# Performance work log

Hardware: AMD Instinct MI355X
Metric: run time of the kernel (lower is better)

## Reference

```python
import jax, jax.numpy as jnp
import numpy as np

NIN = 4096
NOUT = 4096
LN_EPS = 1e-5  # torch.nn.LayerNorm default


def setup_inputs() -> dict:
    key = jax.random.key(0)
    ks = jax.random.split(key, 8)
    x = jax.random.normal(ks[0], (1, NIN), dtype=jnp.float32)
    hid = jax.random.normal(ks[1], (1, NOUT), dtype=jnp.float32)
    hebb = jnp.zeros((NOUT, NOUT), dtype=jnp.float32) + 1e-6  # initialZeroHebb
    # parameters
    w_in = 0.01 * jax.random.normal(ks[2], (NOUT, NIN), dtype=jnp.float32)  # inp_lin weight (no bias)
    w = 0.01 * jnp.eye(NOUT, NOUT, dtype=jnp.float32)                        # Plastic.w
    alpha = 0.01 * jax.random.normal(ks[3], (NOUT, NOUT), dtype=jnp.float32)
    b = 0.01 * jax.random.normal(ks[4], (NOUT,), dtype=jnp.float32)
    lamda = 0.01 * jnp.ones((1,), dtype=jnp.float32)
    pred_eta = 0.01 * jax.random.normal(ks[5], (NOUT, NOUT), dtype=jnp.float32)
    pred_eta_b = 0.01 * jax.random.normal(ks[6], (NOUT,), dtype=jnp.float32)
    ln_gamma = jnp.ones((NOUT,), dtype=jnp.float32)
    ln_beta = jnp.zeros((NOUT,), dtype=jnp.float32)
    return {"x": x, "hid": hid, "hebb": hebb, "w_in": w_in, "w": w,
            "alpha": alpha, "b": b, "lamda": lamda, "pred_eta": pred_eta,
            "pred_eta_b": pred_eta_b, "ln_gamma": ln_gamma, "ln_beta": ln_beta}


def reference(x, hid, hebb, w_in, w, alpha, b, lamda, pred_eta, pred_eta_b, ln_gamma, ln_beta):
    # Cell.forward (nonlin = ReLU for both wx and the post-LN output)
    wx = jax.nn.relu(x @ w_in.T)                       # [1, nout]
    wh = hid @ (w + alpha * hebb) + b                  # Plastic.forward, [1, nout]
    s = wx + wh
    mu = jnp.mean(s, axis=-1, keepdims=True)
    var = jnp.mean((s - mu) ** 2, axis=-1, keepdims=True)
    ln = ln_gamma * (s - mu) * jax.lax.rsqrt(var + LN_EPS) + ln_beta
    wy = jax.nn.relu(ln)                               # new hidden state, [1, nout]
    # Plastic.update_hebb(x=hid, y=wh, hebb)
    eta_hat = jax.nn.sigmoid(wh @ pred_eta + pred_eta_b)           # [1, nout]
    outer = hid[0, :, None] * wh[0, None, :]                        # [nout, nout]
    hebb_new = (1.0 - lamda) * hebb + eta_hat.T * outer             # row i scaled by eta_hat[0, i]
    return wy, hebb_new
```

## Files before the change

kernel.cpp:

```cpp
#include <hip/hip_runtime.h>
#include <hip/hip_bf16.h>
#include <math.h>

#define N 4096
#define NGRP 16

typedef float f32x4 __attribute__((ext_vector_type(4)));

__inline__ __device__ float waveReduceSum(float v) {
    #pragma unroll
    for (int o = 32; o > 0; o >>= 1) v += __shfl_down(v, o);
    return v;
}

#define LD4(p, o) (*reinterpret_cast<const float4*>((p) + (o)))

__inline__ __device__ f32x4 ntld4(const float* p) {
    return __builtin_nontemporal_load(reinterpret_cast<const f32x4*>(p));
}

template<int ITERS>
__global__ __launch_bounds__(256) void k_sweep_wh_t(const float* __restrict__ hid,
                                                    const float* __restrict__ w,
                                                    const float* __restrict__ alpha,
                                                    const float* __restrict__ hebb,
                                                    float* __restrict__ part,
                                                    int G) {
    int b = blockIdx.x, t = threadIdx.x;
    int p = b >> 2;
    int j0 = (((b & 3) << 8) | t) * 4;
    int P = G >> 2;
    size_t step = (size_t)G * 1024;
    size_t off = (size_t)(((b << 8) | t)) * 4;

    f32x4 wv[ITERS], av[ITERS], bv[ITERS];
    float hv[ITERS];
    #pragma unroll
    for (int k = 0; k < ITERS; ++k) {
        size_t o = off + (size_t)k * step;
        wv[k] = ntld4(w + o);
        av[k] = ntld4(alpha + o);
        bv[k] = *reinterpret_cast<const f32x4*>(hebb + o);
    }
    #pragma unroll
    for (int k = 0; k < ITERS; ++k) hv[k] = hid[k * P + p];

    f32x4 acc = {0.f, 0.f, 0.f, 0.f};
    #pragma unroll
    for (int k = 0; k < ITERS; ++k) {
        float h = hv[k];
        acc.x = fmaf(h, fmaf(av[k].x, bv[k].x, wv[k].x), acc.x);
        acc.y = fmaf(h, fmaf(av[k].y, bv[k].y, wv[k].y), acc.y);
        acc.z = fmaf(h, fmaf(av[k].z, bv[k].z, wv[k].z), acc.z);
        acc.w = fmaf(h, fmaf(av[k].w, bv[k].w, wv[k].w), acc.w);
    }
    *reinterpret_cast<f32x4*>(part + (size_t)p * N + j0) = acc;
}

__global__ __launch_bounds__(256) void k_sweep_wh(const float* __restrict__ hid,
                                                  const float* __restrict__ w,
                                                  const float* __restrict__ alpha,
                                                  const float* __restrict__ hebb,
                                                  float* __restrict__ part,
                                                  int G, int iters) {
    int b = blockIdx.x, t = threadIdx.x;
    int p = b >> 2;
    int j0 = (((b & 3) << 8) | t) * 4;
    int P = G >> 2;
    float4 acc = make_float4(0.f, 0.f, 0.f, 0.f);
    size_t step = (size_t)G * 1024;
    size_t off = (size_t)(((b << 8) | t)) * 4;
    #pragma unroll 8
    for (int k = 0; k < iters; ++k, off += step) {
        float h = hid[k * P + p];
        float4 wv = LD4(w, off);
        float4 av = LD4(alpha, off);
        float4 hv = LD4(hebb, off);
        acc.x = fmaf(h, fmaf(av.x, hv.x, wv.x), acc.x);
        acc.y = fmaf(h, fmaf(av.y, hv.y, wv.y), acc.y);
        acc.z = fmaf(h, fmaf(av.z, hv.z, wv.z), acc.z);
        acc.w = fmaf(h, fmaf(av.w, hv.w, wv.w), acc.w);
    }
    *reinterpret_cast<float4*>(part + (size_t)p * N + j0) = acc;
}

__global__ __launch_bounds__(256) void k_red_wx(const float* __restrict__ part,
                                                float* __restrict__ part2,
                                                int cpg,
                                                const float* __restrict__ x,
                                                const float* __restrict__ w_in,
                                                float* __restrict__ wx_out,
                                                int nred) {
    int t = threadIdx.x;
    if ((int)blockIdx.x < nred) {
        int g  = blockIdx.x >> 2;
        int xt = blockIdx.x & 3;
        int j0 = (xt * 256 + t) * 4;
        const float4* p4 = reinterpret_cast<const float4*>(part);
        float4 s = make_float4(0.f, 0.f, 0.f, 0.f);
        #pragma unroll 8
        for (int c = 0; c < cpg; ++c) {
            float4 v = p4[((size_t)(g * cpg + c) * N + j0) >> 2];
            s.x += v.x; s.y += v.y; s.z += v.z; s.w += v.w;
        }
        *reinterpret_cast<float4*>(part2 + (size_t)g * N + j0) = s;
    } else {
        int j = blockIdx.x - nred;
        const float4* row = reinterpret_cast<const float4*>(w_in + (size_t)j * N);
        const float4* xv  = reinterpret_cast<const float4*>(x);
        float sum = 0.f;
        #pragma unroll
        for (int k = t; k < N / 4; k += 256) {
            float4 a = row[k], c = xv[k];
            sum += a.x * c.x + a.y * c.y + a.z * c.z + a.w * c.w;
        }
        sum = waveReduceSum(sum);
        __shared__ float wsum[4];
        int wid = t >> 6, lane = t & 63;
        if (lane == 0) wsum[wid] = sum;
        __syncthreads();
        if (t == 0)
            wx_out[j] = fmaxf(wsum[0] + wsum[1] + wsum[2] + wsum[3], 0.f);
    }
}

__global__ __launch_bounds__(1024) void k_ln(const float* __restrict__ part2,
                                             const float* __restrict__ wx,
                                             const float* __restrict__ b,
                                             const float* __restrict__ gamma,
                                             const float* __restrict__ beta,
                                             float* __restrict__ wh_out,
                                             float* __restrict__ wy_out) {
    __shared__ float red[16];
    __shared__ float bc[2];
    int tid = threadIdx.x;
    int wid = tid >> 6, lane = tid & 63;
    float sv[4];
    float lsum = 0.f;
    #pragma unroll
    for (int q = 0; q < 4; ++q) {
        int j = q * 1024 + tid;
        float acc = b[j];
        #pragma unroll
        for (int g = 0; g < NGRP; ++g) acc += part2[(size_t)g * N + j];
        wh_out[j] = acc;
        float s = acc + wx[j];
        sv[q] = s;
        lsum += s;
    }
    float wv = waveReduceSum(lsum);
    if (lane == 0) red[wid] = wv;
    __syncthreads();
    if (tid < 64) {
        float t = (tid < 16) ? red[tid] : 0.f;
        t = waveReduceSum(t);
        if (tid == 0) bc[0] = t * (1.f / N);
    }
    __syncthreads();
    float mean = bc[0];
    __syncthreads();
    float lsq = 0.f;
    #pragma unroll
    for (int q = 0; q < 4; ++q) { float d = sv[q] - mean; lsq += d * d; }
    wv = waveReduceSum(lsq);
    if (lane == 0) red[wid] = wv;
    __syncthreads();
    if (tid < 64) {
        float t = (tid < 16) ? red[tid] : 0.f;
        t = waveReduceSum(t);
        if (tid == 0) bc[1] = t * (1.f / N);
    }
    __syncthreads();
    float rstd = rsqrtf(bc[1] + 1e-5f);
    #pragma unroll
    for (int q = 0; q < 4; ++q) {
        int j = q * 1024 + tid;
        float ln = fmaf(gamma[j] * (sv[q] - mean), rstd, beta[j]);
        wy_out[j] = fmaxf(ln, 0.f);
    }
}

__global__ __launch_bounds__(1024) void k_eta_hebb(const float* __restrict__ pe,
                                                   const float* __restrict__ pb,
                                                   const float* __restrict__ wh,
                                                   const float* __restrict__ hid,
                                                   const float* __restrict__ lamda,
                                                   const float* __restrict__ hebb,
                                                   float* __restrict__ out) {
    __shared__ float sm[64][17];
    __shared__ float coef_s[16];
    int t  = threadIdx.x;
    int i0 = blockIdx.x * 16;
    int cl = t & 15;
    int g  = t >> 4;
    int c  = i0 + cl;

    float acc = 0.f;
    const float* perow = pe + (size_t)(g * 64) * N + c;
    const float* whp   = wh + g * 64;
    #pragma unroll 8
    for (int k = 0; k < 64; ++k)
        acc = fmaf(whp[k], perow[(size_t)k * N], acc);
    sm[g][cl] = acc;
    __syncthreads();
    #pragma unroll
    for (int off = 32; off >= 1; off >>= 1) {
        if (g < off) sm[g][cl] += sm[g + off][cl];
        __syncthreads();
    }
    if (t < 16) {
        int i = i0 + t;
        float eta = 1.f / (1.f + expf(-(sm[0][t] + pb[i])));
        coef_s[t] = eta * hid[i];
    }
    __syncthreads();

    float decay = 1.f - lamda[0];
    int j = (t & 1023) * 4;
    float4 w4 = LD4(wh, j);
    size_t base = (size_t)i0 * N + j;
    #pragma unroll 4
    for (int r = 0; r < 16; ++r) {
        float coef = coef_s[r];
        float4 h = LD4(hebb, base + (size_t)r * N);
        f32x4 o;
        o.x = fmaf(decay, h.x, coef * w4.x);
        o.y = fmaf(decay, h.y, coef * w4.y);
        o.z = fmaf(decay, h.z, coef * w4.z);
        o.w = fmaf(decay, h.w, coef * w4.w);
        __builtin_nontemporal_store(o, reinterpret_cast<f32x4*>(out + base + (size_t)r * N));
    }
}

extern "C" void kernel_launch(void* const* d_in, const int* in_sizes, int n_in,
                              void* d_out, int out_size, void* d_ws, size_t ws_size,
                              hipStream_t stream) {
    const float* x         = (const float*)d_in[0];
    const float* hid       = (const float*)d_in[1];
    const float* hebb      = (const float*)d_in[2];
    const float* w_in      = (const float*)d_in[3];
    const float* w         = (const float*)d_in[4];
    const float* alpha     = (const float*)d_in[5];
    const float* b         = (const float*)d_in[6];
    const float* lamda     = (const float*)d_in[7];
    const float* pred_eta  = (const float*)d_in[8];
    const float* pred_eta_b= (const float*)d_in[9];
    const float* ln_gamma  = (const float*)d_in[10];
    const float* ln_beta   = (const float*)d_in[11];

    float* wy       = (float*)d_out;
    float* hebb_out = (float*)d_out + N;

    int G = 2048;
    if ((ws_size / 4) < ((size_t)(G / 4) * N + (NGRP + 2) * (size_t)N)) G = 512;
    int P = G / 4;
    int cpg = P / NGRP;
    int nred = 4 * NGRP;

    float* ws    = (float*)d_ws;
    float* part  = ws;
    float* part2 = part + (size_t)P * N;
    float* wx    = part2 + (size_t)NGRP * N;
    float* wh    = wx + N;

    if (G == 2048) {
        k_sweep_wh_t<8><<<G, 256, 0, stream>>>(hid, w, alpha, hebb, part, G);
    } else {
        k_sweep_wh<<<G, 256, 0, stream>>>(hid, w, alpha, hebb, part, G, N * (N / 4) / (G * 256));
    }
    k_red_wx  <<<nred + N, 256, 0, stream>>>(part, part2, cpg, x, w_in, wx, nred);
    k_ln      <<<1, 1024, 0, stream>>>(part2, wx, b, ln_gamma, ln_beta, wh, wy);
    k_eta_hebb<<<256, 1024, 0, stream>>>(pred_eta, pred_eta_b, wh, hid, lamda, hebb, hebb_out);
}
```

Measured before the change: 97.66 us.

## Split eta GEMV into wide coalesced sweep plus fused reduce-and-hebb-update kernel

The wh @ pred_eta GEMV moves out of the hebb-update kernel into its own grid-wide sweep kernel. That kernel uses the same split-K float4 coalesced layout as the wh sweep and writes partial sums to workspace. The hebb kernel then only reduces those partials for its 16 columns before doing the decay/outer-product update. The aim is to stop the 256-block hebb kernel from stalling on strided column reads of the 64MB pred_eta matrix. The cost is one extra launch and a partial-sum round trip through workspace.

```diff
diff --git a/kernel.cpp b/kernel.cpp
--- a/kernel.cpp
+++ b/kernel.cpp
@@ -80,6 +80,60 @@
         acc.y = fmaf(h, fmaf(av.y, hv.y, wv.y), acc.y);
         acc.z = fmaf(h, fmaf(av.z, hv.z, wv.z), acc.z);
         acc.w = fmaf(h, fmaf(av.w, hv.w, wv.w), acc.w);
+    }
+    *reinterpret_cast<float4*>(part + (size_t)p * N + j0) = acc;
+}
+
+template<int ITERS>
+__global__ __launch_bounds__(256) void k_sweep_eta_t(const float* __restrict__ wh,
+                                                     const float* __restrict__ pe,
+                                                     float* __restrict__ part,
+                                                     int G) {
+    int b = blockIdx.x, t = threadIdx.x;
+    int p = b >> 2;
+    int j0 = (((b & 3) << 8) | t) * 4;
+    int P = G >> 2;
+    size_t step = (size_t)G * 1024;
+    size_t off = (size_t)(((b << 8) | t)) * 4;
+
+    f32x4 pv[ITERS];
+    float hv[ITERS];
+    #pragma unroll
+    for (int k = 0; k < ITERS; ++k) pv[k] = *reinterpret_cast<const f32x4*>(pe + off + (size_t)k * step);
+    #pragma unroll
+    for (int k = 0; k < ITERS; ++k) hv[k] = wh[k * P + p];
+
+    f32x4 acc = {0.f, 0.f, 0.f, 0.f};
+    #pragma unroll
+    for (int k = 0; k < ITERS; ++k) {
+        float h = hv[k];
+        acc.x = fmaf(h, pv[k].x, acc.x);
+        acc.y = fmaf(h, pv[k].y, acc.y);
+        acc.z = fmaf(h, pv[k].z, acc.z);
+        acc.w = fmaf(h, pv[k].w, acc.w);
+    }
+    *reinterpret_cast<f32x4*>(part + (size_t)p * N + j0) = acc;
+}
+
+__global__ __launch_bounds__(256) void k_sweep_eta(const float* __restrict__ wh,
+                                                   const float* __restrict__ pe,
+                                                   float* __restrict__ part,
+                                                   int G, int iters) {
+    int b = blockIdx.x, t = threadIdx.x;
+    int p = b >> 2;
+    int j0 = (((b & 3) << 8) | t) * 4;
+    int P = G >> 2;
+    float4 acc = make_float4(0.f, 0.f, 0.f, 0.f);
+    size_t step = (size_t)G * 1024;
+    size_t off = (size_t)(((b << 8) | t)) * 4;
+    #pragma unroll 8
+    for (int k = 0; k < iters; ++k, off += step) {
+        float h = wh[k * P + p];
+        float4 pv = LD4(pe, off);
+        acc.x = fmaf(h, pv.x, acc.x);
+        acc.y = fmaf(h, pv.y, acc.y);
+        acc.z = fmaf(h, pv.z, acc.z);
+        acc.w = fmaf(h, pv.w, acc.w);
     }
     *reinterpret_cast<float4*>(part + (size_t)p * N + j0) = acc;
 }
@@ -180,32 +234,30 @@
     }
 }
 
-__global__ __launch_bounds__(1024) void k_eta_hebb(const float* __restrict__ pe,
-                                                   const float* __restrict__ pb,
-                                                   const float* __restrict__ wh,
-                                                   const float* __restrict__ hid,
-                                                   const float* __restrict__ lamda,
-                                                   const float* __restrict__ hebb,
-                                                   float* __restrict__ out) {
+__global__ __launch_bounds__(1024) void k_redfin_hebb(const float* __restrict__ part,
+                                                      const float* __restrict__ pb,
+                                                      const float* __restrict__ wh,
+                                                      const float* __restrict__ hid,
+                                                      const float* __restrict__ lamda,
+                                                      const float* __restrict__ hebb,
+                                                      float* __restrict__ out,
+                                                      int P) {
     __shared__ float sm[64][17];
     __shared__ float coef_s[16];
     int t  = threadIdx.x;
     int i0 = blockIdx.x * 16;
-    int cl = t & 15;
-    int g  = t >> 4;
-    int c  = i0 + cl;
-
-    float acc = 0.f;
-    const float* perow = pe + (size_t)(g * 64) * N + c;
-    const float* whp   = wh + g * 64;
-    #pragma unroll 8
-    for (int k = 0; k < 64; ++k)
-        acc = fmaf(whp[k], perow[(size_t)k * N], acc);
-    sm[g][cl] = acc;
+    int il = t & 15;
+    int ps = t >> 4;
+    int q  = P >> 6;
+
+    float s = 0.f;
+    for (int k = 0; k < q; ++k)
+        s += part[(size_t)(ps * q + k) * N + i0 + il];
+    sm[ps][il] = s;
     __syncthreads();
     #pragma unroll
     for (int off = 32; off >= 1; off >>= 1) {
-        if (g < off) sm[g][cl] += sm[g + off][cl];
+        if (ps < off) sm[ps][il] += sm[ps + off][il];
         __syncthreads();
     }
     if (t < 16) {
@@ -216,7 +268,7 @@
     __syncthreads();
 
     float decay = 1.f - lamda[0];
-    int j = (t & 1023) * 4;
+    int j = t * 4;
     float4 w4 = LD4(wh, j);
     size_t base = (size_t)i0 * N + j;
     #pragma unroll 4
@@ -255,6 +307,7 @@
     if ((ws_size / 4) < ((size_t)(G / 4) * N + (NGRP + 2) * (size_t)N)) G = 512;
     int P = G / 4;
     int cpg = P / NGRP;
+    int iters = (N * (N / 4)) / (G * 256);
     int nred = 4 * NGRP;
 
     float* ws    = (float*)d_ws;
@@ -266,9 +319,14 @@
     if (G == 2048) {
         k_sweep_wh_t<8><<<G, 256, 0, stream>>>(hid, w, alpha, hebb, part, G);
     } else {
-        k_sweep_wh<<<G, 256, 0, stream>>>(hid, w, alpha, hebb, part, G, N * (N / 4) / (G * 256));
-    }
-    k_red_wx  <<<nred + N, 256, 0, stream>>>(part, part2, cpg, x, w_in, wx, nred);
-    k_ln      <<<1, 1024, 0, stream>>>(part2, wx, b, ln_gamma, ln_beta, wh, wy);
-    k_eta_hebb<<<256, 1024, 0, stream>>>(pred_eta, pred_eta_b, wh, hid, lamda, hebb, hebb_out);
-}
+        k_sweep_wh<<<G, 256, 0, stream>>>(hid, w, alpha, hebb, part, G, iters);
+    }
+    k_red_wx<<<nred + N, 256, 0, stream>>>(part, part2, cpg, x, w_in, wx, nred);
+    k_ln    <<<1, 1024, 0, stream>>>(part2, wx, b, ln_gamma, ln_beta, wh, wy);
+    if (G == 2048) {
+        k_sweep_eta_t<8><<<G, 256, 0, stream>>>(wh, pred_eta, part, G);
+    } else {
+        k_sweep_eta<<<G, 256, 0, stream>>>(wh, pred_eta, part, G, iters);
+    }
+    k_redfin_hebb<<<256, 1024, 0, stream>>>(part, pred_eta_b, wh, hid, lamda, hebb, hebb_out, P);
+}
```

Result: no change. 97.28 us (-0.4%).
